# Kernel optimization log

Measured on AMD Instinct MI355X. Metric: run time of the kernel, lower is better.

The kernel has to match this reference:

```python
import jax, jax.numpy as jnp
import numpy as np


def setup_inputs() -> dict:
    key = jax.random.key(0)
    kq, kk, kv, ki, ks = jax.random.split(key, 5)
    B, H, S, D, VD, T = 2, 8, 2048, 64, 64, 128
    q = jax.random.normal(kq, (B, H, S, D), dtype=jnp.float32)
    k = jax.random.normal(kk, (B, H, S, D), dtype=jnp.float32)
    v = jax.random.normal(kv, (B, H, S, VD), dtype=jnp.float32)
    topk_indices = jax.random.randint(ki, (B, S, T), 0, S, dtype=jnp.int64)
    topk_scores = jax.random.uniform(ks, (B, S, T), dtype=jnp.float32)
    return {"q": q, "k": k, "v": v, "topk_indices": topk_indices,
            "topk_scores": topk_scores}


def reference(q, k, v, topk_indices, topk_scores):
    # q: (B,H,S,D), k: (B,H,S,D), v: (B,H,S,VD), topk_indices: (B,S,T)
    head_dim = q.shape[-1]
    scale = head_dim ** (-0.5)

    # Gather selected K/V per query directly (no O(S^2) expansion).
    # For each batch b: kb (H,S,D), idx (S,T) -> kb[:, idx, :] (H,S,T,D)
    gather = jax.vmap(lambda xb, ib: xb[:, ib, :])
    k_g = gather(k, topk_indices)  # (B,H,S,T,D)
    v_g = gather(v, topk_indices)  # (B,H,S,T,VD)

    # (B,H,S,T) scores
    attn_scores = jnp.einsum('bhsd,bhstd->bhst', q, k_g) * scale
    attn_weights = jax.nn.softmax(attn_scores, axis=-1)

    # reweight by indexer scores (broadcast over heads), then renormalize
    attn_weights = attn_weights * topk_scores[:, None, :, :]
    attn_weights = attn_weights / (attn_weights.sum(axis=-1, keepdims=True) + 1e-12)

    # (B,H,S,VD)
    output = jnp.einsum('bhst,bhstd->bhsd', attn_weights, v_g)
    return output
```

## Files before the change

kernel.cpp:

```cpp
#include <hip/hip_runtime.h>
#include <math.h>


#define BB 2
#define HH 8
#define SS 2048
#define DD 64
#define VDD 64
#define TT 128
#define SCALE 0.125f
#define LOG2E 1.44269504088896340736f
#define NKV (BB * HH * SS * DD)

typedef __fp16 h2 __attribute__((ext_vector_type(2)));
typedef float  f2 __attribute__((ext_vector_type(2)));

__device__ __forceinline__ float bf_lo(unsigned int u) {
    return __uint_as_float(u << 16);
}
__device__ __forceinline__ float bf_hi(unsigned int u) {
    return __uint_as_float(u);
}
__device__ __forceinline__ unsigned short f2bf_rne(float f) {
    unsigned int u = __float_as_uint(f);
    u += 0x7FFFu + ((u >> 16) & 1u);
    return (unsigned short)(u >> 16);
}
__device__ __forceinline__ unsigned int pk_f16(float x, float y) {
    h2 p = __builtin_amdgcn_cvt_pkrtz(x, y);
    return __builtin_bit_cast(unsigned int, p);
}
__device__ __forceinline__ float dot2(unsigned int qh, unsigned int kh, float c) {
    return __builtin_amdgcn_fdot2(__builtin_bit_cast(h2, qh),
                                  __builtin_bit_cast(h2, kh), c, false);
}

__global__ __launch_bounds__(256) void cvt_kv(
    const float* __restrict__ k, const float* __restrict__ v,
    unsigned int* __restrict__ kh, unsigned int* __restrict__ vb)
{
    int i = (blockIdx.x * 256 + threadIdx.x) * 4;
    if (i >= NKV) return;
    float4 kf = *(const float4*)(k + i);
    float4 vf = *(const float4*)(v + i);
    unsigned int k0 = pk_f16(kf.x, kf.y);
    unsigned int k1 = pk_f16(kf.z, kf.w);
    unsigned int v0 = (unsigned int)f2bf_rne(vf.x) | ((unsigned int)f2bf_rne(vf.y) << 16);
    unsigned int v1 = (unsigned int)f2bf_rne(vf.z) | ((unsigned int)f2bf_rne(vf.w) << 16);
    *(uint2*)(kh + i / 2) = make_uint2(k0, k1);
    *(uint2*)(vb + i / 2) = make_uint2(v0, v1);
}

__global__ __launch_bounds__(256, 4) void dsa_sparse_attn_bf16(
    const float* __restrict__ q,
    const unsigned int* __restrict__ kh,
    const unsigned int* __restrict__ vb,
    const int* __restrict__ topk_idx,
    const float* __restrict__ topk_sc,
    float* __restrict__ out)
{
    const int tid  = threadIdx.x;
    const int wave = tid >> 6;
    const int lane = tid & 63;
    const int h    = lane & 7;
    const int g    = lane >> 3;

    const int plane = blockIdx.x & 15;
    const int s     = (blockIdx.x >> 4) * 4 + wave;
    const int b     = plane >> 3;

    const float*        qp  = q  + ((size_t)plane * SS + s) * DD;
    const unsigned int* kp  = kh + (size_t)plane * SS * (DD / 2);
    const unsigned int* vp  = vb + (size_t)plane * SS * (VDD / 2);
    const int*          ip  = topk_idx + ((size_t)b * SS + s) * TT;
    const float*        scp = topk_sc  + ((size_t)b * SS + s) * TT;
    float*              op  = out + ((size_t)plane * SS + s) * VDD;

    int   iv0 = ip[lane];
    int   iv1 = ip[64 + lane];
    float sv0 = scp[lane];
    float sv1 = scp[64 + lane];
    float4 qa = *(const float4*)(qp + h * 8);
    float4 qb = *(const float4*)(qp + h * 8 + 4);
    const float QS = SCALE * LOG2E;
    unsigned int q0 = pk_f16(qa.x * QS, qa.y * QS);
    unsigned int q1 = pk_f16(qa.z * QS, qa.w * QS);
    unsigned int q2 = pk_f16(qb.x * QS, qb.y * QS);
    unsigned int q3 = pk_f16(qb.z * QS, qb.w * QS);

    float m   = -1e30f;
    float sum = 0.f;
    f2 a0 = {0.f, 0.f}, a1 = {0.f, 0.f}, a2 = {0.f, 0.f}, a3 = {0.f, 0.f};

    #pragma unroll
    for (int tc = 0; tc < 8; ++tc) {
        int   idx = __shfl(iv0, tc * 8 + g);
        float sc  = __shfl(sv0, tc * 8 + g);
        uint4 kk  = *(const uint4*)(kp + (size_t)idx * 32 + h * 4);
        uint4 vv  = *(const uint4*)(vp + (size_t)idx * 32 + h * 4);
        float st  = dot2(q0, kk.x, dot2(q1, kk.y, dot2(q2, kk.z, dot2(q3, kk.w, 0.f))));
        st += __shfl_xor(st, 1);
        st += __shfl_xor(st, 2);
        st += __shfl_xor(st, 4);
        float mn = fmaxf(m, st);
        float r  = exp2f(m - mn);
        float e  = exp2f(st - mn) * sc;
        m = mn;
        sum = fmaf(sum, r, e);
        f2 rv = {r, r}, ev = {e, e};
        f2 vx = {bf_lo(vv.x), bf_hi(vv.x)};
        f2 vy = {bf_lo(vv.y), bf_hi(vv.y)};
        f2 vz = {bf_lo(vv.z), bf_hi(vv.z)};
        f2 vw = {bf_lo(vv.w), bf_hi(vv.w)};
        a0 = __builtin_elementwise_fma(a0, rv, ev * vx);
        a1 = __builtin_elementwise_fma(a1, rv, ev * vy);
        a2 = __builtin_elementwise_fma(a2, rv, ev * vz);
        a3 = __builtin_elementwise_fma(a3, rv, ev * vw);
    }
    #pragma unroll
    for (int tc = 0; tc < 8; ++tc) {
        int   idx = __shfl(iv1, tc * 8 + g);
        float sc  = __shfl(sv1, tc * 8 + g);
        uint4 kk  = *(const uint4*)(kp + (size_t)idx * 32 + h * 4);
        uint4 vv  = *(const uint4*)(vp + (size_t)idx * 32 + h * 4);
        float st  = dot2(q0, kk.x, dot2(q1, kk.y, dot2(q2, kk.z, dot2(q3, kk.w, 0.f))));
        st += __shfl_xor(st, 1);
        st += __shfl_xor(st, 2);
        st += __shfl_xor(st, 4);
        float mn = fmaxf(m, st);
        float r  = exp2f(m - mn);
        float e  = exp2f(st - mn) * sc;
        m = mn;
        sum = fmaf(sum, r, e);
        f2 rv = {r, r}, ev = {e, e};
        f2 vx = {bf_lo(vv.x), bf_hi(vv.x)};
        f2 vy = {bf_lo(vv.y), bf_hi(vv.y)};
        f2 vz = {bf_lo(vv.z), bf_hi(vv.z)};
        f2 vw = {bf_lo(vv.w), bf_hi(vv.w)};
        a0 = __builtin_elementwise_fma(a0, rv, ev * vx);
        a1 = __builtin_elementwise_fma(a1, rv, ev * vy);
        a2 = __builtin_elementwise_fma(a2, rv, ev * vz);
        a3 = __builtin_elementwise_fma(a3, rv, ev * vw);
    }

    float a[8] = {a0.x, a0.y, a1.x, a1.y, a2.x, a2.y, a3.x, a3.y};
    #pragma unroll
    for (int off = 8; off <= 32; off <<= 1) {
        float m2 = __shfl_xor(m, off);
        float s2 = __shfl_xor(sum, off);
        float mn = fmaxf(m, m2);
        float r1 = exp2f(m - mn);
        float r2 = exp2f(m2 - mn);
        sum = sum * r1 + s2 * r2;
        #pragma unroll
        for (int j = 0; j < 8; ++j) {
            float o = __shfl_xor(a[j], off);
            a[j] = a[j] * r1 + o * r2;
        }
        m = mn;
    }

    if (g == 0) {
        float inv = 1.0f / (sum + 1e-12f);
        *(float4*)(op + h * 8)     = make_float4(a[0] * inv, a[1] * inv, a[2] * inv, a[3] * inv);
        *(float4*)(op + h * 8 + 4) = make_float4(a[4] * inv, a[5] * inv, a[6] * inv, a[7] * inv);
    }
}

__global__ __launch_bounds__(256, 4) void dsa_sparse_attn_f32(
    const float* __restrict__ q,
    const float* __restrict__ k,
    const float* __restrict__ v,
    const int* __restrict__ topk_idx,
    const float* __restrict__ topk_sc,
    float* __restrict__ out)
{
    const int tid  = threadIdx.x;
    const int wave = tid >> 6;
    const int lane = tid & 63;
    const int plane = blockIdx.x & 15;
    const int s     = (blockIdx.x >> 4) * 4 + wave;
    const int b     = plane >> 3;

    const float* qp  = q + ((size_t)plane * SS + s) * DD;
    const float* kp  = k + (size_t)plane * SS * DD;
    const float* vp  = v + (size_t)plane * SS * VDD;
    const int*   ip  = topk_idx + ((size_t)b * SS + s) * TT;
    const float* scp = topk_sc  + ((size_t)b * SS + s) * TT;
    float*       op  = out + ((size_t)plane * SS + s) * VDD;

    __shared__ int   s_idx[4][TT];
    __shared__ float s_w[4][TT];

    float sc0 = scp[lane];
    float sc1 = scp[64 + lane];
    s_idx[wave][lane]      = ip[lane];
    s_idx[wave][64 + lane] = ip[64 + lane];

    const int l = lane & 3;
    const int g = lane >> 2;
    float4 qf[4];
    #pragma unroll
    for (int j = 0; j < 4; ++j) qf[j] = *(const float4*)(qp + l * 4 + 16 * j);
    __syncthreads();

    #pragma unroll
    for (int tc = 0; tc < 8; ++tc) {
        int t = tc * 16 + g;
        const float* krow = kp + (size_t)s_idx[wave][t] * DD;
        float acc = 0.f;
        #pragma unroll
        for (int j = 0; j < 4; ++j) {
            float4 kf = *(const float4*)(krow + l * 4 + 16 * j);
            acc += qf[j].x * kf.x + qf[j].y * kf.y + qf[j].z * kf.z + qf[j].w * kf.w;
        }
        acc += __shfl_xor(acc, 1);
        acc += __shfl_xor(acc, 2);
        if (l == 0) s_w[wave][t] = acc * SCALE;
    }
    __syncthreads();

    float a0 = s_w[wave][lane];
    float a1 = s_w[wave][64 + lane];
    float m = fmaxf(a0, a1);
    #pragma unroll
    for (int off = 32; off >= 1; off >>= 1) m = fmaxf(m, __shfl_xor(m, off));
    float e0 = __expf(a0 - m) * sc0;
    float e1 = __expf(a1 - m) * sc1;
    float sum = e0 + e1;
    #pragma unroll
    for (int off = 32; off >= 1; off >>= 1) sum += __shfl_xor(sum, off);
    float inv = 1.0f / (sum + 1e-12f);
    s_w[wave][lane]      = e0 * inv;
    s_w[wave][64 + lane] = e1 * inv;
    __syncthreads();

    float acc = 0.f;
    #pragma unroll 8
    for (int t = 0; t < TT; ++t)
        acc = fmaf(s_w[wave][t], vp[(size_t)s_idx[wave][t] * VDD + lane], acc);
    op[lane] = acc;
}

extern "C" void kernel_launch(void* const* d_in, const int* in_sizes, int n_in,
                              void* d_out, int out_size, void* d_ws, size_t ws_size,
                              hipStream_t stream) {
    const float* q   = (const float*)d_in[0];
    const float* k   = (const float*)d_in[1];
    const float* v   = (const float*)d_in[2];
    const int*   idx = (const int*)d_in[3];
    const float* sc  = (const float*)d_in[4];
    float*       out = (float*)d_out;

    const size_t need = (size_t)NKV * 2 * 2;
    if (ws_size >= need) {
        unsigned int* kh = (unsigned int*)d_ws;
        unsigned int* vb = kh + NKV / 2;
        hipLaunchKernelGGL(cvt_kv, dim3(NKV / 4 / 256), dim3(256), 0, stream,
                           k, v, kh, vb);
        hipLaunchKernelGGL(dsa_sparse_attn_bf16, dim3(8192), dim3(256), 0, stream,
                           q, kh, vb, idx, sc, out);
    } else {
        hipLaunchKernelGGL(dsa_sparse_attn_f32, dim3(8192), dim3(256), 0, stream,
                           q, k, v, idx, sc, out);
    }
}
```

Baseline: 130.9 us.

## Split sparse attention into two-pass scores then PV without online softmax

Splits the bf16 kernel into two phases. The first computes all 128 QK scores with 4 lanes per key row and takes a global max and sum over the wave. The second accumulates PV with the final softmax weights, so the per-step rescaling and the exp work of online softmax go away. It also makes the end-of-kernel cross-group merge a plain sum instead of a max-rescale merge. In exchange it adds extra shuffles to redistribute weights and holds more score registers.

```diff
diff --git a/kernel.cpp b/kernel.cpp
--- a/kernel.cpp
+++ b/kernel.cpp
@@ -62,6 +62,8 @@
     const int tid  = threadIdx.x;
     const int wave = tid >> 6;
     const int lane = tid & 63;
+    const int l    = lane & 3;
+    const int r    = lane >> 2;
     const int h    = lane & 7;
     const int g    = lane >> 3;
 
@@ -80,88 +82,112 @@
     int   iv1 = ip[64 + lane];
     float sv0 = scp[lane];
     float sv1 = scp[64 + lane];
-    float4 qa = *(const float4*)(qp + h * 8);
-    float4 qb = *(const float4*)(qp + h * 8 + 4);
+    float4 qA0 = *(const float4*)(qp + l * 8);
+    float4 qA1 = *(const float4*)(qp + l * 8 + 4);
+    float4 qB0 = *(const float4*)(qp + 32 + l * 8);
+    float4 qB1 = *(const float4*)(qp + 32 + l * 8 + 4);
     const float QS = SCALE * LOG2E;
-    unsigned int q0 = pk_f16(qa.x * QS, qa.y * QS);
-    unsigned int q1 = pk_f16(qa.z * QS, qa.w * QS);
-    unsigned int q2 = pk_f16(qb.x * QS, qb.y * QS);
-    unsigned int q3 = pk_f16(qb.z * QS, qb.w * QS);
-
-    float m   = -1e30f;
+    unsigned int qa0 = pk_f16(qA0.x * QS, qA0.y * QS);
+    unsigned int qa1 = pk_f16(qA0.z * QS, qA0.w * QS);
+    unsigned int qa2 = pk_f16(qA1.x * QS, qA1.y * QS);
+    unsigned int qa3 = pk_f16(qA1.z * QS, qA1.w * QS);
+    unsigned int qb0 = pk_f16(qB0.x * QS, qB0.y * QS);
+    unsigned int qb1 = pk_f16(qB0.z * QS, qB0.w * QS);
+    unsigned int qb2 = pk_f16(qB1.x * QS, qB1.y * QS);
+    unsigned int qb3 = pk_f16(qB1.z * QS, qB1.w * QS);
+
+    float sco[8];
+    #pragma unroll
+    for (int tc = 0; tc < 4; ++tc) {
+        int idx = __shfl(iv0, tc * 16 + r);
+        const unsigned int* row = kp + (size_t)idx * 32;
+        uint4 k0 = *(const uint4*)(row + l * 4);
+        uint4 k1 = *(const uint4*)(row + 16 + l * 4);
+        float st = dot2(qa0, k0.x, dot2(qa1, k0.y, dot2(qa2, k0.z, dot2(qa3, k0.w, 0.f))));
+        st = dot2(qb0, k1.x, dot2(qb1, k1.y, dot2(qb2, k1.z, dot2(qb3, k1.w, st))));
+        st += __shfl_xor(st, 1);
+        st += __shfl_xor(st, 2);
+        sco[tc] = st;
+    }
+    #pragma unroll
+    for (int tc = 0; tc < 4; ++tc) {
+        int idx = __shfl(iv1, tc * 16 + r);
+        const unsigned int* row = kp + (size_t)idx * 32;
+        uint4 k0 = *(const uint4*)(row + l * 4);
+        uint4 k1 = *(const uint4*)(row + 16 + l * 4);
+        float st = dot2(qa0, k0.x, dot2(qa1, k0.y, dot2(qa2, k0.z, dot2(qa3, k0.w, 0.f))));
+        st = dot2(qb0, k1.x, dot2(qb1, k1.y, dot2(qb2, k1.z, dot2(qb3, k1.w, st))));
+        st += __shfl_xor(st, 1);
+        st += __shfl_xor(st, 2);
+        sco[4 + tc] = st;
+    }
+
+    float m = sco[0];
+    #pragma unroll
+    for (int tc = 1; tc < 8; ++tc) m = fmaxf(m, sco[tc]);
+    m = fmaxf(m, __shfl_xor(m, 4));
+    m = fmaxf(m, __shfl_xor(m, 8));
+    m = fmaxf(m, __shfl_xor(m, 16));
+    m = fmaxf(m, __shfl_xor(m, 32));
     float sum = 0.f;
+    #pragma unroll
+    for (int tc = 0; tc < 4; ++tc) {
+        float e = exp2f(sco[tc] - m) * __shfl(sv0, tc * 16 + r);
+        sco[tc] = e;
+        sum += e;
+    }
+    #pragma unroll
+    for (int tc = 0; tc < 4; ++tc) {
+        float e = exp2f(sco[4 + tc] - m) * __shfl(sv1, tc * 16 + r);
+        sco[4 + tc] = e;
+        sum += e;
+    }
+    sum += __shfl_xor(sum, 4);
+    sum += __shfl_xor(sum, 8);
+    sum += __shfl_xor(sum, 16);
+    sum += __shfl_xor(sum, 32);
+    float inv = 1.0f / (sum + 1e-12f);
+
     f2 a0 = {0.f, 0.f}, a1 = {0.f, 0.f}, a2 = {0.f, 0.f}, a3 = {0.f, 0.f};
-
     #pragma unroll
     for (int tc = 0; tc < 8; ++tc) {
         int   idx = __shfl(iv0, tc * 8 + g);
-        float sc  = __shfl(sv0, tc * 8 + g);
-        uint4 kk  = *(const uint4*)(kp + (size_t)idx * 32 + h * 4);
+        float e   = __shfl(sco[tc >> 1], ((tc & 1) * 8 + g) * 4);
         uint4 vv  = *(const uint4*)(vp + (size_t)idx * 32 + h * 4);
-        float st  = dot2(q0, kk.x, dot2(q1, kk.y, dot2(q2, kk.z, dot2(q3, kk.w, 0.f))));
-        st += __shfl_xor(st, 1);
-        st += __shfl_xor(st, 2);
-        st += __shfl_xor(st, 4);
-        float mn = fmaxf(m, st);
-        float r  = exp2f(m - mn);
-        float e  = exp2f(st - mn) * sc;
-        m = mn;
-        sum = fmaf(sum, r, e);
-        f2 rv = {r, r}, ev = {e, e};
+        f2 ev = {e, e};
         f2 vx = {bf_lo(vv.x), bf_hi(vv.x)};
         f2 vy = {bf_lo(vv.y), bf_hi(vv.y)};
         f2 vz = {bf_lo(vv.z), bf_hi(vv.z)};
         f2 vw = {bf_lo(vv.w), bf_hi(vv.w)};
-        a0 = __builtin_elementwise_fma(a0, rv, ev * vx);
-        a1 = __builtin_elementwise_fma(a1, rv, ev * vy);
-        a2 = __builtin_elementwise_fma(a2, rv, ev * vz);
-        a3 = __builtin_elementwise_fma(a3, rv, ev * vw);
+        a0 = __builtin_elementwise_fma(ev, vx, a0);
+        a1 = __builtin_elementwise_fma(ev, vy, a1);
+        a2 = __builtin_elementwise_fma(ev, vz, a2);
+        a3 = __builtin_elementwise_fma(ev, vw, a3);
     }
     #pragma unroll
     for (int tc = 0; tc < 8; ++tc) {
         int   idx = __shfl(iv1, tc * 8 + g);
-        float sc  = __shfl(sv1, tc * 8 + g);
-        uint4 kk  = *(const uint4*)(kp + (size_t)idx * 32 + h * 4);
+        float e   = __shfl(sco[4 + (tc >> 1)], ((tc & 1) * 8 + g) * 4);
         uint4 vv  = *(const uint4*)(vp + (size_t)idx * 32 + h * 4);
-        float st  = dot2(q0, kk.x, dot2(q1, kk.y, dot2(q2, kk.z, dot2(q3, kk.w, 0.f))));
-        st += __shfl_xor(st, 1);
-        st += __shfl_xor(st, 2);
-        st += __shfl_xor(st, 4);
-        float mn = fmaxf(m, st);
-        float r  = exp2f(m - mn);
-        float e  = exp2f(st - mn) * sc;
-        m = mn;
-        sum = fmaf(sum, r, e);
-        f2 rv = {r, r}, ev = {e, e};
+        f2 ev = {e, e};
         f2 vx = {bf_lo(vv.x), bf_hi(vv.x)};
         f2 vy = {bf_lo(vv.y), bf_hi(vv.y)};
         f2 vz = {bf_lo(vv.z), bf_hi(vv.z)};
         f2 vw = {bf_lo(vv.w), bf_hi(vv.w)};
-        a0 = __builtin_elementwise_fma(a0, rv, ev * vx);
-        a1 = __builtin_elementwise_fma(a1, rv, ev * vy);
-        a2 = __builtin_elementwise_fma(a2, rv, ev * vz);
-        a3 = __builtin_elementwise_fma(a3, rv, ev * vw);
+        a0 = __builtin_elementwise_fma(ev, vx, a0);
+        a1 = __builtin_elementwise_fma(ev, vy, a1);
+        a2 = __builtin_elementwise_fma(ev, vz, a2);
+        a3 = __builtin_elementwise_fma(ev, vw, a3);
     }
 
     float a[8] = {a0.x, a0.y, a1.x, a1.y, a2.x, a2.y, a3.x, a3.y};
     #pragma unroll
-    for (int off = 8; off <= 32; off <<= 1) {
-        float m2 = __shfl_xor(m, off);
-        float s2 = __shfl_xor(sum, off);
-        float mn = fmaxf(m, m2);
-        float r1 = exp2f(m - mn);
-        float r2 = exp2f(m2 - mn);
-        sum = sum * r1 + s2 * r2;
-        #pragma unroll
-        for (int j = 0; j < 8; ++j) {
-            float o = __shfl_xor(a[j], off);
-            a[j] = a[j] * r1 + o * r2;
-        }
-        m = mn;
-    }
-
+    for (int j = 0; j < 8; ++j) {
+        a[j] += __shfl_xor(a[j], 8);
+        a[j] += __shfl_xor(a[j], 16);
+        a[j] += __shfl_xor(a[j], 32);
+    }
     if (g == 0) {
-        float inv = 1.0f / (sum + 1e-12f);
         *(float4*)(op + h * 8)     = make_float4(a[0] * inv, a[1] * inv, a[2] * inv, a[3] * inv);
         *(float4*)(op + h * 8 + 4) = make_float4(a[4] * inv, a[5] * inv, a[6] * inv, a[7] * inv);
     }
```

Measured after the change: 127.5 us. 2.6% less time.
